# Kernel tuning notes

Hardware: AMD Instinct MI355X
Metric: run time of the kernel (lower is better)

Reference implementation:

```python
import jax, jax.numpy as jnp
import numpy as np

N, E, C, A, F, H = 10000, 160000, 128, 10, 8, 64
AVG_NEIGH = 16.0


def setup_inputs() -> dict:
    key = jax.random.key(0)
    ks = jax.random.split(key, 16)
    inp = {
        "node_attrs": jax.random.uniform(ks[0], (N, A), jnp.float32),
        "node_feats_s": jax.random.normal(ks[1], (N, C), jnp.float32),
        "node_feats_v": jax.random.normal(ks[2], (N, C, 3), jnp.float32),
        "edge_attrs": jax.random.normal(ks[3], (E, 4), jnp.float32),
        "edge_feats": jax.random.normal(ks[4], (E, F), jnp.float32),
        # skip-connection linear after node_feats (x) node_attrs tensor product
        "W_sc_s": jax.random.normal(ks[5], (C * A, C), jnp.float32),
        "W_sc_v": jax.random.normal(ks[6], (C * A, C), jnp.float32),
        # per-l linear on node_feats before the conv TP
        "W_lin_s": jax.random.normal(ks[7], (C, C), jnp.float32),
        "W_lin_v": jax.random.normal(ks[8], (C, C), jnp.float32),
        # radial MLP: 3*[64] + [weight_numel = 5*C]
        "mlp_w0": jax.random.normal(ks[9], (F, H), jnp.float32),
        "mlp_w1": jax.random.normal(ks[10], (H, H), jnp.float32),
        "mlp_w2": jax.random.normal(ks[11], (H, H), jnp.float32),
        "mlp_w3": jax.random.normal(ks[12], (H, 5 * C), jnp.float32),
        # output linear: mid irreps 2Cx0e + 3Cx1o -> Cx0e + Cx1o
        "W_out_s": jax.random.normal(ks[13], (2 * C, C), jnp.float32),
        "W_out_v": jax.random.normal(ks[14], (3 * C, C), jnp.float32),
        "senders": jax.random.randint(ks[15], (E,), 0, N, jnp.int32),
        "receivers": jax.random.randint(jax.random.fold_in(key, 99), (E,), 0, N, jnp.int32),
    }
    return inp


def _forward(node_attrs, node_feats_s, node_feats_v, edge_attrs, edge_feats,
             W_sc_s, W_sc_v, W_lin_s, W_lin_v,
             mlp_w0, mlp_w1, mlp_w2, mlp_w3,
             W_out_s, W_out_v, senders, receivers):
    # --- skip connection: tensor_product(node_feats, node_attrs) then Linear ---
    tp_s = jnp.einsum('nc,na->nca', node_feats_s, node_attrs).reshape(N, C * A)
    tp_v = jnp.einsum('nci,na->ncai', node_feats_v, node_attrs).reshape(N, C * A, 3)
    inv = 1.0 / jnp.sqrt(jnp.float32(C * A))  # e3nn Linear fan-in normalization
    sc_s = (tp_s @ W_sc_s) * inv                               # [N, C]
    sc_v = jnp.einsum('nki,ko->noi', tp_v, W_sc_v) * inv       # [N, C, 3]

    # --- linear on node_feats ---
    invc = 1.0 / jnp.sqrt(jnp.float32(C))
    x_s = (node_feats_s @ W_lin_s) * invc                      # [N, C]
    x_v = jnp.einsum('nci,co->noi', node_feats_v, W_lin_v) * invc  # [N, C, 3]

    # --- radial MLP producing per-edge TP weights (silu hidden, linear out) ---
    h = jax.nn.silu(edge_feats @ mlp_w0 / jnp.sqrt(jnp.float32(F)))
    h = jax.nn.silu(h @ mlp_w1 / jnp.sqrt(jnp.float32(H)))
    h = jax.nn.silu(h @ mlp_w2 / jnp.sqrt(jnp.float32(H)))
    tpw = (h @ mlp_w3) / jnp.sqrt(jnp.float32(H))              # [E, 5C]
    w1, w2, w3, w4, w5 = jnp.split(tpw, 5, axis=-1)            # each [E, C]

    # --- gather sender features ---
    xs = x_s[senders]                                          # [E, C]
    xv = x_v[senders]                                          # [E, C, 3]
    e_s = edge_attrs[:, 0:1]                                   # [E, 1] (0e SH)
    e_v = edge_attrs[:, 1:4]                                   # [E, 3] (1o SH)

    # --- weighted CG tensor product, uvu paths ---
    m0a = w1 * xs * e_s                                        # 0e x 0e -> 0e
    m1a = (w2 * xs)[:, :, None] * e_v[:, None, :]              # 0e x 1o -> 1o
    m1b = w3[:, :, None] * xv * e_s[:, :, None]                # 1o x 0e -> 1o
    m0b = w4 * jnp.einsum('eci,ei->ec', xv, e_v) / jnp.sqrt(3.0)   # 1o x 1o -> 0e
    m1c = w5[:, :, None] * jnp.cross(xv, e_v[:, None, :]) / jnp.sqrt(2.0)  # 1o x 1o -> 1o

    mid_s = jnp.concatenate([m0a, m0b], axis=-1)               # [E, 2C]
    mid_v = jnp.concatenate([m1a, m1b, m1c], axis=1)           # [E, 3C, 3]

    # --- scatter-add messages to receivers ---
    msg_s = jax.ops.segment_sum(mid_s, receivers, num_segments=N)                 # [N, 2C]
    msg_v = jax.ops.segment_sum(mid_v.reshape(E, -1), receivers,
                                num_segments=N).reshape(N, 3 * C, 3)              # [N, 3C, 3]

    # --- output linear / avg_num_neighbors ---
    out_s = (msg_s @ W_out_s) / jnp.sqrt(jnp.float32(2 * C)) / AVG_NEIGH          # [N, C]
    out_v = jnp.einsum('nki,ko->noi', msg_v, W_out_v) / jnp.sqrt(jnp.float32(3 * C)) / AVG_NEIGH

    message = jnp.concatenate([out_s, out_v.reshape(N, C * 3)], axis=-1)  # [N, 4C]
    sc = jnp.concatenate([sc_s, sc_v.reshape(N, C * 3)], axis=-1)         # [N, 4C]
    return message, sc


def reference(node_attrs, node_feats_s, node_feats_v, edge_attrs, edge_feats,
              W_sc_s, W_sc_v, W_lin_s, W_lin_v,
              mlp_w0, mlp_w1, mlp_w2, mlp_w3,
              W_out_s, W_out_v, senders, receivers):
    return _forward(node_attrs, node_feats_s, node_feats_v, edge_attrs, edge_feats,
                    W_sc_s, W_sc_v, W_lin_s, W_lin_v,
                    mlp_w0, mlp_w1, mlp_w2, mlp_w3,
                    W_out_s, W_out_v, senders, receivers)
```

## Files before the change

### kernel.cpp

```cpp
#include <hip/hip_runtime.h>

#define N_NODES 10000
#define N_EDGES 160000

typedef float f32x4 __attribute__((ext_vector_type(4)));
typedef short s8v __attribute__((ext_vector_type(8)));
typedef short s4v __attribute__((ext_vector_type(4)));
typedef unsigned short u4s __attribute__((ext_vector_type(4)));

__device__ __forceinline__ unsigned short f2b(float f) {
    unsigned u = __builtin_bit_cast(unsigned, f);
    u += 0x7FFFu + ((u >> 16) & 1u);
    return (unsigned short)(u >> 16);
}
__device__ __forceinline__ float b2f(unsigned short s) {
    unsigned u = ((unsigned)s) << 16;
    return __builtin_bit_cast(float, u);
}

__global__ void k_prep(const float* s0, const float* s1, const float* s2, const float* s3,
                       const float* s4, const float* s5, const float* s6,
                       const float* s7, const float* s8, const float* nfv, const float* nfs,
                       unsigned short* d0, unsigned short* d1, unsigned short* d2, unsigned short* d3,
                       unsigned short* d4, unsigned short* d5, unsigned short* d6,
                       unsigned short* d7, unsigned short* d8,
                       unsigned short* nfvT, unsigned short* nfsB) {
    int idx = blockIdx.x * 256 + threadIdx.x;
    if (blockIdx.y < 2) {
        const float* src = blockIdx.y ? s1 : s0;
        unsigned short* dst = blockIdx.y ? d1 : d0;
        int k = idx >> 7, o = idx & 127;
        int ci = k / 10, a = k - ci * 10;
        dst[a * 16384 + o * 128 + ci] = f2b(src[idx]);
        return;
    }
    if (blockIdx.y == 9) {
        for (int ch = idx; ch < 960000; ch += 163840) {
            f32x4 v = *reinterpret_cast<const f32x4*>(nfv + (long)ch * 4);
            int f0 = ch * 4;
            int n = f0 / 384, rem = f0 - n * 384;
#pragma unroll
            for (int j = 0; j < 4; j++) {
                int f = rem + j;
                int cc = f / 3, ii = f - cc * 3;
                nfvT[ii * 1280000 + n * 128 + cc] = f2b(v[j]);
            }
        }
        return;
    }
    if (blockIdx.y == 10) {
        for (int ch = idx; ch < 320000; ch += 163840) {
            f32x4 v = *reinterpret_cast<const f32x4*>(nfs + (long)ch * 4);
#pragma unroll
            for (int j = 0; j < 4; j++) nfsB[ch * 4 + j] = f2b(v[j]);
        }
        return;
    }
    const float* src; unsigned short* dst; int K, Nc;
    switch (blockIdx.y) {
        case 2: src = s2; dst = d2; K = 128;  Nc = 128; break;
        case 3: src = s3; dst = d3; K = 128;  Nc = 128; break;
        case 4: src = s4; dst = d4; K = 256;  Nc = 128; break;
        case 5: src = s5; dst = d5; K = 384;  Nc = 128; break;
        case 6: src = s6; dst = d6; K = 64;   Nc = 640; break;
        case 7: src = s7; dst = d7; K = 64;   Nc = 64;  break;
        default: src = s8; dst = d8; K = 64;  Nc = 64;  break;
    }
    if (idx < K * Nc) {
        int k = idx / Nc, c = idx - k * Nc;
        dst[c * K + k] = f2b(src[idx]);
    }
}

__global__ __launch_bounds__(512, 2) void k_sc(const unsigned short* __restrict__ nfsB,
                                               const unsigned short* __restrict__ nfvT,
                                               const float* __restrict__ attr,
                                               const unsigned short* __restrict__ Ws2,
                                               const unsigned short* __restrict__ Wv2,
                                               const unsigned short* __restrict__ wlin_sT,
                                               const unsigned short* __restrict__ wlin_vT,
                                               float* __restrict__ out, float scale,
                                               unsigned short* __restrict__ xpack, float scale2) {
    __shared__ unsigned short As[64][136];
    __shared__ unsigned short Bs[128][140];
    __shared__ float attr_l[64][10];
    const int t = threadIdx.x;
    const int z = blockIdx.y;
    const int row0 = blockIdx.x * 64;
    const int wv = t >> 6, lane = t & 63, lr = lane & 15, lkg = lane >> 4;
    const int wr = (wv & 3) * 16;
    const int wc = (wv >> 2) * 64;

    {
        int r = t >> 3, k0 = (t & 7) * 16;
        int row = row0 + r;
        if (row < N_NODES) {
            const unsigned short* asrc = (z == 0) ? (nfsB + (long)row * 128)
                                                  : (nfvT + (long)(z - 1) * 1280000 + (long)row * 128);
            *reinterpret_cast<s8v*>(&As[r][k0])     = *reinterpret_cast<const s8v*>(asrc + k0);
            *reinterpret_cast<s8v*>(&As[r][k0 + 8]) = *reinterpret_cast<const s8v*>(asrc + k0 + 8);
        } else {
#pragma unroll
            for (int j = 0; j < 16; j++) As[r][k0 + j] = 0;
        }
    }
    for (int idx = t; idx < 640; idx += 512) {
        int r = idx / 10, a = idx - r * 10;
        int row = row0 + r;
        attr_l[r][a] = (row < N_NODES) ? attr[row * 10 + a] : 0.f;
    }
    __syncthreads();

    s8v af[4];
#pragma unroll
    for (int kk = 0; kk < 4; kk++)
        af[kk] = *reinterpret_cast<const s8v*>(&As[wr + lr][kk * 32 + lkg * 8]);

    f32x4 accS[4];
#pragma unroll
    for (int i = 0; i < 4; i++) accS[i] = (f32x4){0.f, 0.f, 0.f, 0.f};

    const unsigned short* Wbase = (z == 0) ? Ws2 : Wv2;
    for (int a = 0; a < 10; a++) {
        {
            const unsigned short* src = Wbase + a * 16384;
            int r = t >> 2, c0 = (t & 3) * 32;
#pragma unroll
            for (int j = 0; j < 4; j++) {
                s8v v = *reinterpret_cast<const s8v*>(src + r * 128 + c0 + j * 8);
                *reinterpret_cast<s8v*>(&Bs[r][c0 + j * 8]) = v;
            }
        }
        __syncthreads();
        f32x4 acc[4];
#pragma unroll
        for (int i = 0; i < 4; i++) acc[i] = (f32x4){0.f, 0.f, 0.f, 0.f};
#pragma unroll
        for (int kk = 0; kk < 4; kk++) {
#pragma unroll
            for (int ct = 0; ct < 4; ct++) {
                s8v bf = *reinterpret_cast<const s8v*>(&Bs[wc + ct * 16 + lr][kk * 32 + lkg * 8]);
                acc[ct] = __builtin_amdgcn_mfma_f32_16x16x32_bf16(af[kk], bf, acc[ct], 0, 0, 0);
            }
        }
#pragma unroll
        for (int r = 0; r < 4; r++) {
            float aw = attr_l[wr + lkg * 4 + r][a];
#pragma unroll
            for (int ct = 0; ct < 4; ct++)
                accS[ct][r] += aw * acc[ct][r];
        }
        __syncthreads();
    }
#pragma unroll
    for (int ct = 0; ct < 4; ct++) {
#pragma unroll
        for (int r = 0; r < 4; r++) {
            int row = row0 + wr + lkg * 4 + r;
            if (row < N_NODES) {
                int col = wc + ct * 16 + lr;
                if (z == 0) out[(long)row * 512 + col] = accS[ct][r] * scale;
                else        out[(long)row * 512 + 128 + col * 3 + (z - 1)] = accS[ct][r] * scale;
            }
        }
    }
    {
        const unsigned short* wl = (z == 0) ? wlin_sT : wlin_vT;
        {
            int r = t >> 2, c0 = (t & 3) * 32;
#pragma unroll
            for (int j = 0; j < 4; j++) {
                s8v v = *reinterpret_cast<const s8v*>(wl + r * 128 + c0 + j * 8);
                *reinterpret_cast<s8v*>(&Bs[r][c0 + j * 8]) = v;
            }
        }
        __syncthreads();
        f32x4 acc[4];
#pragma unroll
        for (int i = 0; i < 4; i++) acc[i] = (f32x4){0.f, 0.f, 0.f, 0.f};
#pragma unroll
        for (int kk = 0; kk < 4; kk++) {
#pragma unroll
            for (int ct = 0; ct < 4; ct++) {
                s8v bf = *reinterpret_cast<const s8v*>(&Bs[wc + ct * 16 + lr][kk * 32 + lkg * 8]);
                acc[ct] = __builtin_amdgcn_mfma_f32_16x16x32_bf16(af[kk], bf, acc[ct], 0, 0, 0);
            }
        }
#pragma unroll
        for (int ct = 0; ct < 4; ct++) {
#pragma unroll
            for (int r = 0; r < 4; r++) {
                int row = row0 + wr + lkg * 4 + r;
                if (row < N_NODES) {
                    int col = wc + ct * 16 + lr;
                    xpack[(long)row * 512 + col * 4 + z] = f2b(acc[ct][r] * scale2);
                }
            }
        }
    }
}

struct GemmZ {
    const float* Ap;
    int ars, aks;
    const unsigned short* Bt;
    float* Cp;
    int crs, ccs;
    int K;
    float scale;
    int M;
    int obf16;
    int abf16;
};

__global__ __launch_bounds__(512, 2) void k_gemm(GemmZ g0, GemmZ g1, GemmZ g2, GemmZ g3) {
    GemmZ g;
    switch (blockIdx.z) { case 0: g = g0; break; case 1: g = g1; break; case 2: g = g2; break; default: g = g3; }
    __shared__ unsigned short As[64][40];
    const int t = threadIdx.x;
    const int wv = t >> 6, lane = t & 63;
    const int lr = lane & 15, lkg = lane >> 4;
    const int row0 = blockIdx.x * 64;
    const int wr = (wv & 3) * 16;
    const int wc = (wv >> 2) * 64;
    const int br = t >> 3;
    const int bk0 = (t & 7) * 4;
    const int arow = row0 + br;

    f32x4 acc[4];
#pragma unroll
    for (int i = 0; i < 4; i++) acc[i] = (f32x4){0.f, 0.f, 0.f, 0.f};

    for (int k0 = 0; k0 < g.K; k0 += 32) {
        s4v av;
        if (arow < g.M) {
            if (g.abf16) {
                const unsigned short* ap = (const unsigned short*)g.Ap + (long)arow * g.ars + k0 + bk0;
                av = *reinterpret_cast<const s4v*>(ap);
            } else if (g.aks == 1) {
                const float* ap = g.Ap + (long)arow * g.ars + k0 + bk0;
                f32x4 v0 = *reinterpret_cast<const f32x4*>(ap);
                av[0] = (short)f2b(v0[0]); av[1] = (short)f2b(v0[1]);
                av[2] = (short)f2b(v0[2]); av[3] = (short)f2b(v0[3]);
            } else {
#pragma unroll
                for (int j = 0; j < 4; j++)
                    av[j] = (short)f2b(g.Ap[(long)arow * g.ars + (long)(k0 + bk0 + j) * g.aks]);
            }
        } else {
#pragma unroll
            for (int j = 0; j < 4; j++) av[j] = 0;
        }
        __syncthreads();
        *reinterpret_cast<s4v*>(&As[br][bk0]) = av;
        __syncthreads();
        s8v af = *reinterpret_cast<const s8v*>(&As[wr + lr][lkg * 8]);
#pragma unroll
        for (int ct = 0; ct < 4; ct++) {
            const unsigned short* bp = g.Bt + (long)(wc + ct * 16 + lr) * g.K + k0 + lkg * 8;
            s8v bf = *reinterpret_cast<const s8v*>(bp);
            acc[ct] = __builtin_amdgcn_mfma_f32_16x16x32_bf16(af, bf, acc[ct], 0, 0, 0);
        }
    }
#pragma unroll
    for (int ct = 0; ct < 4; ct++) {
#pragma unroll
        for (int r = 0; r < 4; r++) {
            int row = row0 + wr + lkg * 4 + r;
            if (row < g.M) {
                int col = wc + ct * 16 + lr;
                if (g.obf16)
                    ((unsigned short*)g.Cp)[(long)row * g.crs + col * g.ccs] = f2b(acc[ct][r] * g.scale);
                else
                    g.Cp[(long)row * g.crs + col * g.ccs] = acc[ct][r] * g.scale;
            }
        }
    }
}

__global__ __launch_bounds__(256) void k_mlp012(const float* __restrict__ ef, const float* __restrict__ w0,
                                                const unsigned short* __restrict__ w1T,
                                                const unsigned short* __restrict__ w2T,
                                                unsigned short* __restrict__ h2out) {
    __shared__ float efs[64][8];
    __shared__ unsigned short hA[64][72];
    __shared__ unsigned short hB[64][72];
    const int t = threadIdx.x;
    const long e0 = (long)blockIdx.x * 64;
#pragma unroll
    for (int j = 0; j < 2; j++) { int idx = t + j * 256; ((float*)efs)[idx] = ef[e0 * 8 + idx]; }
    const int o = t & 63, ebase = t >> 6;
    float w0r[8];
#pragma unroll
    for (int k = 0; k < 8; k++) w0r[k] = w0[k * 64 + o];
    __syncthreads();
#pragma unroll
    for (int j = 0; j < 16; j++) {
        int e = ebase * 16 + j;
        float acc = 0.f;
#pragma unroll
        for (int k = 0; k < 8; k++) acc += efs[e][k] * w0r[k];
        acc *= 0.35355339059f;
        hA[e][o] = f2b(acc / (1.f + __expf(-acc)));
    }
    __syncthreads();
    const int wv = t >> 6, lane = t & 63, lr = lane & 15, lkg = lane >> 4;
    {
        f32x4 acc1[4];
#pragma unroll
        for (int ct = 0; ct < 4; ct++) acc1[ct] = (f32x4){0.f, 0.f, 0.f, 0.f};
#pragma unroll
        for (int kk = 0; kk < 2; kk++) {
            s8v a = *reinterpret_cast<const s8v*>(&hA[wv * 16 + lr][kk * 32 + lkg * 8]);
#pragma unroll
            for (int ct = 0; ct < 4; ct++) {
                s8v b = *reinterpret_cast<const s8v*>(w1T + (ct * 16 + lr) * 64 + kk * 32 + lkg * 8);
                acc1[ct] = __builtin_amdgcn_mfma_f32_16x16x32_bf16(a, b, acc1[ct], 0, 0, 0);
            }
        }
#pragma unroll
        for (int ct = 0; ct < 4; ct++)
#pragma unroll
            for (int r = 0; r < 4; r++) {
                float v = acc1[ct][r] * 0.125f;
                hB[wv * 16 + lkg * 4 + r][ct * 16 + lr] = f2b(v / (1.f + __expf(-v)));
            }
    }
    __syncthreads();
    {
        f32x4 acc2[4];
#pragma unroll
        for (int ct = 0; ct < 4; ct++) acc2[ct] = (f32x4){0.f, 0.f, 0.f, 0.f};
#pragma unroll
        for (int kk = 0; kk < 2; kk++) {
            s8v a = *reinterpret_cast<const s8v*>(&hB[wv * 16 + lr][kk * 32 + lkg * 8]);
#pragma unroll
            for (int ct = 0; ct < 4; ct++) {
                s8v b = *reinterpret_cast<const s8v*>(w2T + (ct * 16 + lr) * 64 + kk * 32 + lkg * 8);
                acc2[ct] = __builtin_amdgcn_mfma_f32_16x16x32_bf16(a, b, acc2[ct], 0, 0, 0);
            }
        }
#pragma unroll
        for (int ct = 0; ct < 4; ct++)
#pragma unroll
            for (int r = 0; r < 4; r++) {
                float v = acc2[ct][r] * 0.125f;
                int row = wv * 16 + lkg * 4 + r;
                h2out[(e0 + row) * 64 + ct * 16 + lr] = f2b(v / (1.f + __expf(-v)));
            }
    }
}

__global__ void k_hist(const int* __restrict__ rcv, int* __restrict__ cnt) {
    int e = blockIdx.x * 256 + threadIdx.x;
    if (e < N_EDGES) atomicAdd(&cnt[rcv[e]], 1);
}

__global__ __launch_bounds__(256) void k_scan(const int* __restrict__ cnt, int* __restrict__ base, int* __restrict__ cur) {
    __shared__ int s[256];
    const int t = threadIdx.x;
    const int c0 = t * 40;
    int sum = 0;
    for (int i = 0; i < 40; i++) sum += cnt[c0 + i];
    s[t] = sum;
    __syncthreads();
    for (int off = 1; off < 256; off <<= 1) {
        int v = (t >= off) ? s[t - off] : 0;
        __syncthreads();
        s[t] += v;
        __syncthreads();
    }
    int run = t ? s[t - 1] : 0;
    for (int i = 0; i < 40; i++) {
        int idx = c0 + i;
        if (idx <= N_NODES) { base[idx] = run; cur[idx] = run; }
        run += cnt[idx];
    }
}

__global__ void k_scatter(const int* __restrict__ rcv, int* __restrict__ cur, int* __restrict__ order) {
    int e = blockIdx.x * 256 + threadIdx.x;
    if (e < N_EDGES) {
        int p = atomicAdd(&cur[rcv[e]], 1);
        order[p] = e;
    }
}

__global__ __launch_bounds__(256, 3) void k_edge2(const unsigned short* __restrict__ h2,
                                                  const unsigned short* __restrict__ w3T,
                                                  const float* __restrict__ eattr,
                                                  const int* __restrict__ snd, const int* __restrict__ rcv,
                                                  const int* __restrict__ order,
                                                  const int* __restrict__ base,
                                                  const unsigned short* __restrict__ xpack,
                                                  float* __restrict__ msg_s, float* __restrict__ msg_v) {
    __shared__ char smem_u[5760];
    __shared__ unsigned short tpwT[640 * 36];
    __shared__ float es_l[32];
    __shared__ float ev_l[32][3];
    __shared__ int sn_l[32], rc_l[32];
    __shared__ int bflags[3];
    unsigned short (*h2s)[72] = (unsigned short(*)[72])smem_u;
    float (*mrg)[11] = (float(*)[11])smem_u;
    const int t = threadIdx.x;
    const int j0 = blockIdx.x * 32;
    {
        int r = t >> 3, kk = (t & 7) * 8;
        int e = order[j0 + r];
        s8v v = *reinterpret_cast<const s8v*>(h2 + (long)e * 64 + kk);
        *reinterpret_cast<s8v*>(&h2s[r][kk]) = v;
    }
    if (t < 32) {
        int e = order[j0 + t];
        es_l[t] = eattr[e * 4 + 0];
        ev_l[t][0] = eattr[e * 4 + 1];
        ev_l[t][1] = eattr[e * 4 + 2];
        ev_l[t][2] = eattr[e * 4 + 3];
        sn_l[t] = snd[e];
        int rc = rcv[e];
        rc_l[t] = rc;
        if (t == 0)  bflags[0] = base[rc];
        if (t == 16) bflags[1] = base[rc];
        if (t == 31) bflags[2] = base[rc + 1];
    }
    __syncthreads();
    const int wv = t >> 6, lane = t & 63, lr = lane & 15, lkg = lane >> 4;
    const int c = t & 127, seg = t >> 7;

    u4s xpr[16];
#pragma unroll
    for (int i = 0; i < 16; i++)
        xpr[i] = *reinterpret_cast<const u4s*>(xpack + (long)sn_l[seg * 16 + i] * 512 + c * 4);

    s8v a00 = *reinterpret_cast<const s8v*>(&h2s[lr][lkg * 8]);
    s8v a01 = *reinterpret_cast<const s8v*>(&h2s[lr][32 + lkg * 8]);
    s8v a10 = *reinterpret_cast<const s8v*>(&h2s[16 + lr][lkg * 8]);
    s8v a11 = *reinterpret_cast<const s8v*>(&h2s[16 + lr][32 + lkg * 8]);
#pragma unroll
    for (int q = 0; q < 10; q++) {
        int co = (wv + 4 * q) * 16 + lr;
        const unsigned short* bp = w3T + (long)co * 64 + lkg * 8;
        s8v b0 = *reinterpret_cast<const s8v*>(bp);
        s8v b1 = *reinterpret_cast<const s8v*>(bp + 32);
        f32x4 ac0 = (f32x4){0.f, 0.f, 0.f, 0.f};
        f32x4 ac1 = (f32x4){0.f, 0.f, 0.f, 0.f};
        ac0 = __builtin_amdgcn_mfma_f32_16x16x32_bf16(a00, b0, ac0, 0, 0, 0);
        ac0 = __builtin_amdgcn_mfma_f32_16x16x32_bf16(a01, b1, ac0, 0, 0, 0);
        ac1 = __builtin_amdgcn_mfma_f32_16x16x32_bf16(a10, b0, ac1, 0, 0, 0);
        ac1 = __builtin_amdgcn_mfma_f32_16x16x32_bf16(a11, b1, ac1, 0, 0, 0);
        u4s p0, p1;
#pragma unroll
        for (int r = 0; r < 4; r++) {
            p0[r] = f2b(ac0[r] * 0.125f);
            p1[r] = f2b(ac1[r] * 0.125f);
        }
        *reinterpret_cast<u4s*>(&tpwT[co * 36 + lkg * 4]) = p0;
        *reinterpret_cast<u4s*>(&tpwT[co * 36 + 16 + lkg * 4]) = p1;
    }
    __syncthreads();

    s4v wsv[5][4];
#pragma unroll
    for (int q = 0; q < 5; q++)
#pragma unroll
        for (int j = 0; j < 4; j++)
            wsv[q][j] = *reinterpret_cast<const s4v*>(&tpwT[(q * 128 + c) * 36 + seg * 16 + j * 4]);

    float A[11], F[11];
#pragma unroll
    for (int q = 0; q < 11; q++) { A[q] = 0.f; F[q] = 0.f; }
    int cur_rc = rc_l[seg * 16];
    int Frc = -1;

#define STORE_RUN(RC, SRC) do { \
        float* ms = msg_s + (long)(RC) * 256 + c; \
        ms[0] = SRC[0]; ms[128] = SRC[1]; \
        float* mv = msg_v + (long)(RC) * 1152 + c; \
        mv[0] = SRC[2]; mv[128] = SRC[3]; mv[256] = SRC[4]; \
        mv[384] = SRC[5]; mv[512] = SRC[6]; mv[640] = SRC[7]; \
        mv[768] = SRC[8]; mv[896] = SRC[9]; mv[1024] = SRC[10]; \
    } while (0)
#define ATOM_RUN(RC, SRC) do { \
        float* ms = msg_s + (long)(RC) * 256 + c; \
        unsafeAtomicAdd(ms, SRC[0]); unsafeAtomicAdd(ms + 128, SRC[1]); \
        float* mv = msg_v + (long)(RC) * 1152 + c; \
        unsafeAtomicAdd(mv + 0, SRC[2]); unsafeAtomicAdd(mv + 128, SRC[3]); \
        unsafeAtomicAdd(mv + 256, SRC[4]); unsafeAtomicAdd(mv + 384, SRC[5]); \
        unsafeAtomicAdd(mv + 512, SRC[6]); unsafeAtomicAdd(mv + 640, SRC[7]); \
        unsafeAtomicAdd(mv + 768, SRC[8]); unsafeAtomicAdd(mv + 896, SRC[9]); \
        unsafeAtomicAdd(mv + 1024, SRC[10]); \
    } while (0)

#pragma unroll
    for (int i = 0; i < 16; i++) {
        int idx = seg * 16 + i;
        int rc = rc_l[idx];
        if (rc != cur_rc) {
            if (Frc < 0) {
#pragma unroll
                for (int q = 0; q < 11; q++) { F[q] = A[q]; A[q] = 0.f; }
                Frc = cur_rc;
            } else {
                STORE_RUN(cur_rc, A);
#pragma unroll
                for (int q = 0; q < 11; q++) A[q] = 0.f;
            }
            cur_rc = rc;
        }
        float es = es_l[idx], ev0 = ev_l[idx][0], ev1 = ev_l[idx][1], ev2 = ev_l[idx][2];
        float w1 = b2f((unsigned short)wsv[0][i >> 2][i & 3]);
        float w2 = b2f((unsigned short)wsv[1][i >> 2][i & 3]);
        float w3 = b2f((unsigned short)wsv[2][i >> 2][i & 3]);
        float w4 = b2f((unsigned short)wsv[3][i >> 2][i & 3]);
        float w5 = b2f((unsigned short)wsv[4][i >> 2][i & 3]);
        float xsv = b2f(xpr[i][0]);
        float x0 = b2f(xpr[i][1]), x1 = b2f(xpr[i][2]), x2 = b2f(xpr[i][3]);
        A[0] += w1 * xsv * es;
        float dve = x0 * ev0 + x1 * ev1 + x2 * ev2;
        A[1] += w4 * dve * 0.57735026919f;
        float a2 = w2 * xsv;
        A[2] += a2 * ev0;
        A[3] += w3 * x0 * es;
        A[4] += w5 * (x1 * ev2 - x2 * ev1) * 0.70710678119f;
        A[5] += a2 * ev1;
        A[6] += w3 * x1 * es;
        A[7] += w5 * (x2 * ev0 - x0 * ev2) * 0.70710678119f;
        A[8] += a2 * ev2;
        A[9] += w3 * x2 * es;
        A[10] += w5 * (x0 * ev1 - x1 * ev0) * 0.70710678119f;
    }
    const bool merge = (rc_l[15] == rc_l[16]);
    if (seg == 0) {
        if (merge) {
#pragma unroll
            for (int q = 0; q < 11; q++) mrg[c][q] = A[q];
            if (Frc >= 0) {
                if (bflags[0] == j0) STORE_RUN(Frc, F); else ATOM_RUN(Frc, F);
            }
        } else {
            if (Frc < 0) {
                if (bflags[0] == j0) STORE_RUN(cur_rc, A); else ATOM_RUN(cur_rc, A);
            } else {
                if (bflags[0] == j0) STORE_RUN(Frc, F); else ATOM_RUN(Frc, F);
                STORE_RUN(cur_rc, A);
            }
        }
    } else {
        if (!merge) {
            if (Frc < 0) {
                if (bflags[2] == j0 + 32) STORE_RUN(cur_rc, A); else ATOM_RUN(cur_rc, A);
            } else {
                STORE_RUN(Frc, F);
                if (bflags[2] == j0 + 32) STORE_RUN(cur_rc, A); else ATOM_RUN(cur_rc, A);
            }
        }
    }
    __syncthreads();
    if (seg == 1 && merge) {
        if (Frc < 0) {
#pragma unroll
            for (int q = 0; q < 11; q++) A[q] += mrg[c][q];
            bool st = (bflags[1] >= j0) && (bflags[2] == j0 + 32);
            if (st) STORE_RUN(cur_rc, A); else ATOM_RUN(cur_rc, A);
        } else {
#pragma unroll
            for (int q = 0; q < 11; q++) F[q] += mrg[c][q];
            if (bflags[1] >= j0) STORE_RUN(Frc, F); else ATOM_RUN(Frc, F);
            if (bflags[2] == j0 + 32) STORE_RUN(cur_rc, A); else ATOM_RUN(cur_rc, A);
        }
    }
#undef STORE_RUN
#undef ATOM_RUN
}

extern "C" void kernel_launch(void* const* d_in, const int* in_sizes, int n_in,
                              void* d_out, int out_size, void* d_ws, size_t ws_size,
                              hipStream_t stream) {
    const float* node_attrs = (const float*)d_in[0];
    const float* nfs        = (const float*)d_in[1];
    const float* nfv        = (const float*)d_in[2];
    const float* edge_attrs = (const float*)d_in[3];
    const float* edge_feats = (const float*)d_in[4];
    const float* W_sc_s     = (const float*)d_in[5];
    const float* W_sc_v     = (const float*)d_in[6];
    const float* W_lin_s    = (const float*)d_in[7];
    const float* W_lin_v    = (const float*)d_in[8];
    const float* mlp_w0     = (const float*)d_in[9];
    const float* mlp_w1     = (const float*)d_in[10];
    const float* mlp_w2     = (const float*)d_in[11];
    const float* mlp_w3     = (const float*)d_in[12];
    const float* W_out_s    = (const float*)d_in[13];
    const float* W_out_v    = (const float*)d_in[14];
    const int* senders      = (const int*)d_in[15];
    const int* receivers    = (const int*)d_in[16];
    float* dout = (float*)d_out;

    char* W = (char*)d_ws;
    unsigned short* xpack_ws = (unsigned short*)(W + 0);
    float* msgs_ws = (float*)(W + 10240000);
    float* msgv_ws = (float*)(W + 20480000);
    unsigned short* nfvT_ws = (unsigned short*)(W + 20480000);
    unsigned short* nfsB_ws = (unsigned short*)(W + 28160000);
    unsigned short* h2_ws   = (unsigned short*)(W + 66560000);
    unsigned short* wsc_s2  = (unsigned short*)(W + 87040000);
    unsigned short* wsc_v2  = (unsigned short*)(W + 87367680);
    unsigned short* wlin_sT = (unsigned short*)(W + 87695360);
    unsigned short* wlin_vT = (unsigned short*)(W + 87728128);
    unsigned short* wout_sT = (unsigned short*)(W + 87760896);
    unsigned short* wout_vT = (unsigned short*)(W + 87826432);
    unsigned short* w3T     = (unsigned short*)(W + 87924736);
    unsigned short* w1T     = (unsigned short*)(W + 88006656);
    unsigned short* w2T     = (unsigned short*)(W + 88014848);
    int* cnt_ws   = (int*)(W + 88023040);
    int* base_ws  = (int*)(W + 88064000);
    int* cur_ws   = (int*)(W + 88104960);
    int* order_ws = (int*)(W + 88145920);

    const float inv1280 = 0.02795084972f;
    const float inv128  = 0.08838834765f;
    const float scO_s   = 1.f / 256.f;
    const float scO_v   = 1.f / (19.5959179423f * 16.f);

    k_prep<<<dim3(640, 11, 1), 256, 0, stream>>>(W_sc_s, W_sc_v, W_lin_s, W_lin_v, W_out_s, W_out_v, mlp_w3,
                                                 mlp_w1, mlp_w2, nfv, nfs,
                                                 wsc_s2, wsc_v2, wlin_sT, wlin_vT, wout_sT, wout_vT, w3T,
                                                 w1T, w2T, nfvT_ws, nfsB_ws);
    k_mlp012<<<dim3(2500), 256, 0, stream>>>(edge_feats, mlp_w0, w1T, w2T, h2_ws);

    k_sc<<<dim3(157, 4), 512, 0, stream>>>(nfsB_ws, nfvT_ws, node_attrs, wsc_s2, wsc_v2,
                                           wlin_sT, wlin_vT, dout + 5120000, inv1280,
                                           xpack_ws, inv128);

    hipMemsetAsync(msgs_ws, 0, 56320000, stream);
    hipMemsetAsync(cnt_ws, 0, 40960, stream);
    k_hist<<<dim3(625), 256, 0, stream>>>(receivers, cnt_ws);
    k_scan<<<dim3(1), 256, 0, stream>>>(cnt_ws, base_ws, cur_ws);
    k_scatter<<<dim3(625), 256, 0, stream>>>(receivers, cur_ws, order_ws);
    k_edge2<<<dim3(5000), 256, 0, stream>>>(h2_ws, w3T, edge_attrs, senders, receivers, order_ws,
                                            base_ws, xpack_ws, msgs_ws, msgv_ws);

    {
        GemmZ g0{msgs_ws,       256,  1, wout_sT, dout,           512, 1, 256, scO_s, N_NODES, 0, 0};
        GemmZ g1{msgv_ws + 0,   1152, 1, wout_vT, dout + 128 + 0, 512, 3, 384, scO_v, N_NODES, 0, 0};
        GemmZ g2{msgv_ws + 384, 1152, 1, wout_vT, dout + 128 + 1, 512, 3, 384, scO_v, N_NODES, 0, 0};
        GemmZ g3{msgv_ws + 768, 1152, 1, wout_vT, dout + 128 + 2, 512, 3, 384, scO_v, N_NODES, 0, 0};
        k_gemm<<<dim3(157, 1, 4), 512, 0, stream>>>(g0, g1, g2, g3);
    }
}
```

Baseline: 282.5 us.

## Merge skip-connection GEMM, radial MLP and receiver histogram into one launch

Three independent front-end kernels (skip-connection/linear GEMM, the first radial MLP layers, and the receiver histogram) are combined into a single horizontally fused kernel that dispatches on block index. The MLP part now uses 512-thread blocks over 128 edges, and the counter memset is moved ahead of the prep kernel. The aim is to cut launch overhead and let these small, underfilling stages share the GPU concurrently. In exchange every role gets the same shared-memory footprint and register budget, which may lower occupancy for the lighter MLP and histogram blocks.

```diff
diff --git a/kernel.cpp b/kernel.cpp
--- a/kernel.cpp
+++ b/kernel.cpp
@@ -72,119 +72,105 @@
     }
 }
 
-__global__ __launch_bounds__(512, 2) void k_sc(const unsigned short* __restrict__ nfsB,
-                                               const unsigned short* __restrict__ nfvT,
-                                               const float* __restrict__ attr,
-                                               const unsigned short* __restrict__ Ws2,
-                                               const unsigned short* __restrict__ Wv2,
-                                               const unsigned short* __restrict__ wlin_sT,
-                                               const unsigned short* __restrict__ wlin_vT,
-                                               float* __restrict__ out, float scale,
-                                               unsigned short* __restrict__ xpack, float scale2) {
-    __shared__ unsigned short As[64][136];
-    __shared__ unsigned short Bs[128][140];
-    __shared__ float attr_l[64][10];
+#define NB_SC 628
+#define NB_MLP 1250
+#define NB_HIST 313
+
+__global__ __launch_bounds__(512, 2) void k_front(const unsigned short* __restrict__ nfsB,
+                                                  const unsigned short* __restrict__ nfvT,
+                                                  const float* __restrict__ attr,
+                                                  const unsigned short* __restrict__ Ws2,
+                                                  const unsigned short* __restrict__ Wv2,
+                                                  const unsigned short* __restrict__ wlin_sT,
+                                                  const unsigned short* __restrict__ wlin_vT,
+                                                  float* __restrict__ out, float scale,
+                                                  unsigned short* __restrict__ xpack, float scale2,
+                                                  const float* __restrict__ ef,
+                                                  const float* __restrict__ w0,
+                                                  const unsigned short* __restrict__ w1T,
+                                                  const unsigned short* __restrict__ w2T,
+                                                  unsigned short* __restrict__ h2out,
+                                                  const int* __restrict__ rcv,
+                                                  int* __restrict__ cnt) {
+    __shared__ char sm[55808];
     const int t = threadIdx.x;
-    const int z = blockIdx.y;
-    const int row0 = blockIdx.x * 64;
+    const int bid = blockIdx.x;
     const int wv = t >> 6, lane = t & 63, lr = lane & 15, lkg = lane >> 4;
-    const int wr = (wv & 3) * 16;
-    const int wc = (wv >> 2) * 64;
-
-    {
-        int r = t >> 3, k0 = (t & 7) * 16;
-        int row = row0 + r;
-        if (row < N_NODES) {
-            const unsigned short* asrc = (z == 0) ? (nfsB + (long)row * 128)
-                                                  : (nfvT + (long)(z - 1) * 1280000 + (long)row * 128);
-            *reinterpret_cast<s8v*>(&As[r][k0])     = *reinterpret_cast<const s8v*>(asrc + k0);
-            *reinterpret_cast<s8v*>(&As[r][k0 + 8]) = *reinterpret_cast<const s8v*>(asrc + k0 + 8);
-        } else {
-#pragma unroll
-            for (int j = 0; j < 16; j++) As[r][k0 + j] = 0;
-        }
-    }
-    for (int idx = t; idx < 640; idx += 512) {
-        int r = idx / 10, a = idx - r * 10;
-        int row = row0 + r;
-        attr_l[r][a] = (row < N_NODES) ? attr[row * 10 + a] : 0.f;
-    }
-    __syncthreads();
-
-    s8v af[4];
-#pragma unroll
-    for (int kk = 0; kk < 4; kk++)
-        af[kk] = *reinterpret_cast<const s8v*>(&As[wr + lr][kk * 32 + lkg * 8]);
-
-    f32x4 accS[4];
-#pragma unroll
-    for (int i = 0; i < 4; i++) accS[i] = (f32x4){0.f, 0.f, 0.f, 0.f};
-
-    const unsigned short* Wbase = (z == 0) ? Ws2 : Wv2;
-    for (int a = 0; a < 10; a++) {
+
+    if (bid >= NB_SC + NB_MLP) {
+        int e = (bid - NB_SC - NB_MLP) * 512 + t;
+        if (e < N_EDGES) atomicAdd(&cnt[rcv[e]], 1);
+        return;
+    }
+
+    if (bid < NB_SC) {
+        unsigned short (*As)[136] = (unsigned short(*)[136])(sm);
+        unsigned short (*Bs)[140] = (unsigned short(*)[140])(sm + 17408);
+        float (*attr_l)[10] = (float(*)[10])(sm + 53248);
+        const int z = bid & 3;
+        const int row0 = (bid >> 2) * 64;
+        const int wr = (wv & 3) * 16;
+        const int wc = (wv >> 2) * 64;
         {
-            const unsigned short* src = Wbase + a * 16384;
-            int r = t >> 2, c0 = (t & 3) * 32;
-#pragma unroll
-            for (int j = 0; j < 4; j++) {
-                s8v v = *reinterpret_cast<const s8v*>(src + r * 128 + c0 + j * 8);
-                *reinterpret_cast<s8v*>(&Bs[r][c0 + j * 8]) = v;
-            }
-        }
-        __syncthreads();
-        f32x4 acc[4];
-#pragma unroll
-        for (int i = 0; i < 4; i++) acc[i] = (f32x4){0.f, 0.f, 0.f, 0.f};
-#pragma unroll
-        for (int kk = 0; kk < 4; kk++) {
-#pragma unroll
-            for (int ct = 0; ct < 4; ct++) {
-                s8v bf = *reinterpret_cast<const s8v*>(&Bs[wc + ct * 16 + lr][kk * 32 + lkg * 8]);
-                acc[ct] = __builtin_amdgcn_mfma_f32_16x16x32_bf16(af[kk], bf, acc[ct], 0, 0, 0);
-            }
-        }
-#pragma unroll
-        for (int r = 0; r < 4; r++) {
-            float aw = attr_l[wr + lkg * 4 + r][a];
-#pragma unroll
-            for (int ct = 0; ct < 4; ct++)
-                accS[ct][r] += aw * acc[ct][r];
-        }
-        __syncthreads();
-    }
-#pragma unroll
-    for (int ct = 0; ct < 4; ct++) {
-#pragma unroll
-        for (int r = 0; r < 4; r++) {
-            int row = row0 + wr + lkg * 4 + r;
+            int r = t >> 3, k0 = (t & 7) * 16;
+            int row = row0 + r;
             if (row < N_NODES) {
-                int col = wc + ct * 16 + lr;
-                if (z == 0) out[(long)row * 512 + col] = accS[ct][r] * scale;
-                else        out[(long)row * 512 + 128 + col * 3 + (z - 1)] = accS[ct][r] * scale;
-            }
-        }
-    }
-    {
-        const unsigned short* wl = (z == 0) ? wlin_sT : wlin_vT;
-        {
-            int r = t >> 2, c0 = (t & 3) * 32;
-#pragma unroll
-            for (int j = 0; j < 4; j++) {
-                s8v v = *reinterpret_cast<const s8v*>(wl + r * 128 + c0 + j * 8);
-                *reinterpret_cast<s8v*>(&Bs[r][c0 + j * 8]) = v;
-            }
-        }
-        __syncthreads();
-        f32x4 acc[4];
-#pragma unroll
-        for (int i = 0; i < 4; i++) acc[i] = (f32x4){0.f, 0.f, 0.f, 0.f};
-#pragma unroll
-        for (int kk = 0; kk < 4; kk++) {
-#pragma unroll
-            for (int ct = 0; ct < 4; ct++) {
-                s8v bf = *reinterpret_cast<const s8v*>(&Bs[wc + ct * 16 + lr][kk * 32 + lkg * 8]);
-                acc[ct] = __builtin_amdgcn_mfma_f32_16x16x32_bf16(af[kk], bf, acc[ct], 0, 0, 0);
-            }
+                const unsigned short* asrc = (z == 0) ? (nfsB + (long)row * 128)
+                                                      : (nfvT + (long)(z - 1) * 1280000 + (long)row * 128);
+                *reinterpret_cast<s8v*>(&As[r][k0])     = *reinterpret_cast<const s8v*>(asrc + k0);
+                *reinterpret_cast<s8v*>(&As[r][k0 + 8]) = *reinterpret_cast<const s8v*>(asrc + k0 + 8);
+            } else {
+#pragma unroll
+                for (int j = 0; j < 16; j++) As[r][k0 + j] = 0;
+            }
+        }
+        for (int idx = t; idx < 640; idx += 512) {
+            int r = idx / 10, a = idx - r * 10;
+            int row = row0 + r;
+            attr_l[r][a] = (row < N_NODES) ? attr[row * 10 + a] : 0.f;
+        }
+        __syncthreads();
+
+        s8v af[4];
+#pragma unroll
+        for (int kk = 0; kk < 4; kk++)
+            af[kk] = *reinterpret_cast<const s8v*>(&As[wr + lr][kk * 32 + lkg * 8]);
+
+        f32x4 accS[4];
+#pragma unroll
+        for (int i = 0; i < 4; i++) accS[i] = (f32x4){0.f, 0.f, 0.f, 0.f};
+
+        const unsigned short* Wbase = (z == 0) ? Ws2 : Wv2;
+        for (int a = 0; a < 10; a++) {
+            {
+                const unsigned short* src = Wbase + a * 16384;
+                int r = t >> 2, c0 = (t & 3) * 32;
+#pragma unroll
+                for (int j = 0; j < 4; j++) {
+                    s8v v = *reinterpret_cast<const s8v*>(src + r * 128 + c0 + j * 8);
+                    *reinterpret_cast<s8v*>(&Bs[r][c0 + j * 8]) = v;
+                }
+            }
+            __syncthreads();
+            f32x4 acc[4];
+#pragma unroll
+            for (int i = 0; i < 4; i++) acc[i] = (f32x4){0.f, 0.f, 0.f, 0.f};
+#pragma unroll
+            for (int kk = 0; kk < 4; kk++) {
+#pragma unroll
+                for (int ct = 0; ct < 4; ct++) {
+                    s8v bf = *reinterpret_cast<const s8v*>(&Bs[wc + ct * 16 + lr][kk * 32 + lkg * 8]);
+                    acc[ct] = __builtin_amdgcn_mfma_f32_16x16x32_bf16(af[kk], bf, acc[ct], 0, 0, 0);
+                }
+            }
+#pragma unroll
+            for (int r = 0; r < 4; r++) {
+                float aw = attr_l[wr + lkg * 4 + r][a];
+#pragma unroll
+                for (int ct = 0; ct < 4; ct++)
+                    accS[ct][r] += aw * acc[ct][r];
+            }
+            __syncthreads();
         }
 #pragma unroll
         for (int ct = 0; ct < 4; ct++) {
@@ -193,9 +179,113 @@
                 int row = row0 + wr + lkg * 4 + r;
                 if (row < N_NODES) {
                     int col = wc + ct * 16 + lr;
-                    xpack[(long)row * 512 + col * 4 + z] = f2b(acc[ct][r] * scale2);
-                }
-            }
+                    if (z == 0) out[(long)row * 512 + col] = accS[ct][r] * scale;
+                    else        out[(long)row * 512 + 128 + col * 3 + (z - 1)] = accS[ct][r] * scale;
+                }
+            }
+        }
+        {
+            const unsigned short* wl = (z == 0) ? wlin_sT : wlin_vT;
+            {
+                int r = t >> 2, c0 = (t & 3) * 32;
+#pragma unroll
+                for (int j = 0; j < 4; j++) {
+                    s8v v = *reinterpret_cast<const s8v*>(wl + r * 128 + c0 + j * 8);
+                    *reinterpret_cast<s8v*>(&Bs[r][c0 + j * 8]) = v;
+                }
+            }
+            __syncthreads();
+            f32x4 acc[4];
+#pragma unroll
+            for (int i = 0; i < 4; i++) acc[i] = (f32x4){0.f, 0.f, 0.f, 0.f};
+#pragma unroll
+            for (int kk = 0; kk < 4; kk++) {
+#pragma unroll
+                for (int ct = 0; ct < 4; ct++) {
+                    s8v bf = *reinterpret_cast<const s8v*>(&Bs[wc + ct * 16 + lr][kk * 32 + lkg * 8]);
+                    acc[ct] = __builtin_amdgcn_mfma_f32_16x16x32_bf16(af[kk], bf, acc[ct], 0, 0, 0);
+                }
+            }
+#pragma unroll
+            for (int ct = 0; ct < 4; ct++) {
+#pragma unroll
+                for (int r = 0; r < 4; r++) {
+                    int row = row0 + wr + lkg * 4 + r;
+                    if (row < N_NODES) {
+                        int col = wc + ct * 16 + lr;
+                        xpack[(long)row * 512 + col * 4 + z] = f2b(acc[ct][r] * scale2);
+                    }
+                }
+            }
+        }
+        return;
+    }
+
+    {
+        float (*efs)[8] = (float(*)[8])(sm);
+        unsigned short (*hA)[72] = (unsigned short(*)[72])(sm + 4096);
+        unsigned short (*hB)[72] = (unsigned short(*)[72])(sm + 22528);
+        const long e0 = (long)(bid - NB_SC) * 128;
+#pragma unroll
+        for (int j = 0; j < 2; j++) { int idx = t + j * 512; ((float*)efs)[idx] = ef[e0 * 8 + idx]; }
+        const int o = t & 63, ebase = t >> 6;
+        float w0r[8];
+#pragma unroll
+        for (int k = 0; k < 8; k++) w0r[k] = w0[k * 64 + o];
+        __syncthreads();
+#pragma unroll
+        for (int j = 0; j < 16; j++) {
+            int e = ebase * 16 + j;
+            float acc = 0.f;
+#pragma unroll
+            for (int k = 0; k < 8; k++) acc += efs[e][k] * w0r[k];
+            acc *= 0.35355339059f;
+            hA[e][o] = f2b(acc / (1.f + __expf(-acc)));
+        }
+        __syncthreads();
+        {
+            f32x4 acc1[4];
+#pragma unroll
+            for (int ct = 0; ct < 4; ct++) acc1[ct] = (f32x4){0.f, 0.f, 0.f, 0.f};
+#pragma unroll
+            for (int kk = 0; kk < 2; kk++) {
+                s8v a = *reinterpret_cast<const s8v*>(&hA[wv * 16 + lr][kk * 32 + lkg * 8]);
+#pragma unroll
+                for (int ct = 0; ct < 4; ct++) {
+                    s8v b = *reinterpret_cast<const s8v*>(w1T + (ct * 16 + lr) * 64 + kk * 32 + lkg * 8);
+                    acc1[ct] = __builtin_amdgcn_mfma_f32_16x16x32_bf16(a, b, acc1[ct], 0, 0, 0);
+                }
+            }
+#pragma unroll
+            for (int ct = 0; ct < 4; ct++)
+#pragma unroll
+                for (int r = 0; r < 4; r++) {
+                    float v = acc1[ct][r] * 0.125f;
+                    hB[wv * 16 + lkg * 4 + r][ct * 16 + lr] = f2b(v / (1.f + __expf(-v)));
+                }
+        }
+        __syncthreads();
+        {
+            f32x4 acc2[4];
+#pragma unroll
+            for (int ct = 0; ct < 4; ct++) acc2[ct] = (f32x4){0.f, 0.f, 0.f, 0.f};
+#pragma unroll
+            for (int kk = 0; kk < 2; kk++) {
+                s8v a = *reinterpret_cast<const s8v*>(&hB[wv * 16 + lr][kk * 32 + lkg * 8]);
+#pragma unroll
+                for (int ct = 0; ct < 4; ct++) {
+                    s8v b = *reinterpret_cast<const s8v*>(w2T + (ct * 16 + lr) * 64 + kk * 32 + lkg * 8);
+                    acc2[ct] = __builtin_amdgcn_mfma_f32_16x16x32_bf16(a, b, acc2[ct], 0, 0, 0);
+                }
+            }
+#pragma unroll
+            for (int ct = 0; ct < 4; ct++)
+#pragma unroll
+                for (int r = 0; r < 4; r++) {
+                    float v = acc2[ct][r] * 0.125f;
+                    int row = wv * 16 + lkg * 4 + r;
+                    h2out[(e0 + row) * 64 + ct * 16 + lr] = f2b(v / (1.f + __expf(-v)));
+                }
         }
     }
 }
@@ -276,84 +366,6 @@
             }
         }
     }
-}
-
-__global__ __launch_bounds__(256) void k_mlp012(const float* __restrict__ ef, const float* __restrict__ w0,
-                                                const unsigned short* __restrict__ w1T,
-                                                const unsigned short* __restrict__ w2T,
-                                                unsigned short* __restrict__ h2out) {
-    __shared__ float efs[64][8];
-    __shared__ unsigned short hA[64][72];
-    __shared__ unsigned short hB[64][72];
-    const int t = threadIdx.x;
-    const long e0 = (long)blockIdx.x * 64;
-#pragma unroll
-    for (int j = 0; j < 2; j++) { int idx = t + j * 256; ((float*)efs)[idx] = ef[e0 * 8 + idx]; }
-    const int o = t & 63, ebase = t >> 6;
-    float w0r[8];
-#pragma unroll
-    for (int k = 0; k < 8; k++) w0r[k] = w0[k * 64 + o];
-    __syncthreads();
-#pragma unroll
-    for (int j = 0; j < 16; j++) {
-        int e = ebase * 16 + j;
-        float acc = 0.f;
-#pragma unroll
-        for (int k = 0; k < 8; k++) acc += efs[e][k] * w0r[k];
-        acc *= 0.35355339059f;
-        hA[e][o] = f2b(acc / (1.f + __expf(-acc)));
-    }
-    __syncthreads();
-    const int wv = t >> 6, lane = t & 63, lr = lane & 15, lkg = lane >> 4;
-    {
-        f32x4 acc1[4];
-#pragma unroll
-        for (int ct = 0; ct < 4; ct++) acc1[ct] = (f32x4){0.f, 0.f, 0.f, 0.f};
-#pragma unroll
-        for (int kk = 0; kk < 2; kk++) {
-            s8v a = *reinterpret_cast<const s8v*>(&hA[wv * 16 + lr][kk * 32 + lkg * 8]);
-#pragma unroll
-            for (int ct = 0; ct < 4; ct++) {
-                s8v b = *reinterpret_cast<const s8v*>(w1T + (ct * 16 + lr) * 64 + kk * 32 + lkg * 8);
-                acc1[ct] = __builtin_amdgcn_mfma_f32_16x16x32_bf16(a, b, acc1[ct], 0, 0, 0);
-            }
-        }
-#pragma unroll
-        for (int ct = 0; ct < 4; ct++)
-#pragma unroll
-            for (int r = 0; r < 4; r++) {
-                float v = acc1[ct][r] * 0.125f;
-                hB[wv * 16 + lkg * 4 + r][ct * 16 + lr] = f2b(v / (1.f + __expf(-v)));
-            }
-    }
-    __syncthreads();
-    {
-        f32x4 acc2[4];
-#pragma unroll
-        for (int ct = 0; ct < 4; ct++) acc2[ct] = (f32x4){0.f, 0.f, 0.f, 0.f};
-#pragma unroll
-        for (int kk = 0; kk < 2; kk++) {
-            s8v a = *reinterpret_cast<const s8v*>(&hB[wv * 16 + lr][kk * 32 + lkg * 8]);
-#pragma unroll
-            for (int ct = 0; ct < 4; ct++) {
-                s8v b = *reinterpret_cast<const s8v*>(w2T + (ct * 16 + lr) * 64 + kk * 32 + lkg * 8);
-                acc2[ct] = __builtin_amdgcn_mfma_f32_16x16x32_bf16(a, b, acc2[ct], 0, 0, 0);
-            }
-        }
-#pragma unroll
-        for (int ct = 0; ct < 4; ct++)
-#pragma unroll
-            for (int r = 0; r < 4; r++) {
-                float v = acc2[ct][r] * 0.125f;
-                int row = wv * 16 + lkg * 4 + r;
-                h2out[(e0 + row) * 64 + ct * 16 + lr] = f2b(v / (1.f + __expf(-v)));
-            }
-    }
-}
-
-__global__ void k_hist(const int* __restrict__ rcv, int* __restrict__ cnt) {
-    int e = blockIdx.x * 256 + threadIdx.x;
-    if (e < N_EDGES) atomicAdd(&cnt[rcv[e]], 1);
 }
 
 __global__ __launch_bounds__(256) void k_scan(const int* __restrict__ cnt, int* __restrict__ base, int* __restrict__ cur) {
@@ -621,19 +633,19 @@
     const float scO_s   = 1.f / 256.f;
     const float scO_v   = 1.f / (19.5959179423f * 16.f);
 
+    hipMemsetAsync(cnt_ws, 0, 40960, stream);
     k_prep<<<dim3(640, 11, 1), 256, 0, stream>>>(W_sc_s, W_sc_v, W_lin_s, W_lin_v, W_out_s, W_out_v, mlp_w3,
                                                  mlp_w1, mlp_w2, nfv, nfs,
                                                  wsc_s2, wsc_v2, wlin_sT, wlin_vT, wout_sT, wout_vT, w3T,
                                                  w1T, w2T, nfvT_ws, nfsB_ws);
-    k_mlp012<<<dim3(2500), 256, 0, stream>>>(edge_feats, mlp_w0, w1T, w2T, h2_ws);
-
-    k_sc<<<dim3(157, 4), 512, 0, stream>>>(nfsB_ws, nfvT_ws, node_attrs, wsc_s2, wsc_v2,
-                                           wlin_sT, wlin_vT, dout + 5120000, inv1280,
-                                           xpack_ws, inv128);
+
+    k_front<<<dim3(NB_SC + NB_MLP + NB_HIST), 512, 0, stream>>>(
+        nfsB_ws, nfvT_ws, node_attrs, wsc_s2, wsc_v2, wlin_sT, wlin_vT,
+        dout + 5120000, inv1280, xpack_ws, inv128,
+        edge_feats, mlp_w0, w1T, w2T, h2_ws,
+        receivers, cnt_ws);
 
     hipMemsetAsync(msgs_ws, 0, 56320000, stream);
-    hipMemsetAsync(cnt_ws, 0, 40960, stream);
-    k_hist<<<dim3(625), 256, 0, stream>>>(receivers, cnt_ws);
     k_scan<<<dim3(1), 256, 0, stream>>>(cnt_ws, base_ws, cur_ws);
     k_scatter<<<dim3(625), 256, 0, stream>>>(receivers, cur_ws, order_ws);
     k_edge2<<<dim3(5000), 256, 0, stream>>>(h2_ws, w3T, edge_attrs, senders, receivers, order_ws,
```

New measurement: 373.8 us. 32.3% more time.
